# Kernel optimization log

Measured on AMD Instinct MI355X. Metric: run time of the kernel, lower is better.

Reference implementation:

```python
import jax, jax.numpy as jnp
import numpy as np

# dims matching init_kwargs
B, S, D, DH, E, K = 16, 8192, 256, 512, 8, 2


def setup_inputs() -> dict:
    key = jax.random.key(0)
    k0, k1, k2, k3 = jax.random.split(key, 4)
    scale = 0.02
    x = jax.random.normal(k0, (B, S, D), dtype=jnp.float32)
    gate_w = jax.random.normal(k1, (E, D), dtype=jnp.float32) * scale   # Linear(d_model, E, bias=False): weight [E, D]
    w1 = jax.random.normal(k2, (E, DH, D), dtype=jnp.float32) * scale   # fc1 weight per expert [DH, D]
    b1 = jnp.zeros((E, DH), dtype=jnp.float32)
    w2 = jax.random.normal(k3, (E, D, DH), dtype=jnp.float32) * scale   # fc2 weight per expert [D, DH]
    b2 = jnp.zeros((E, D), dtype=jnp.float32)
    return {"x": x, "gate_w": gate_w, "w1": w1, "b1": b1, "w2": w2, "b2": b2}


def reference(x, gate_w, w1, b1, w2, b2):
    b, s, d = x.shape
    e = gate_w.shape[0]
    xf = x.reshape(-1, d)                      # [T, D]
    T = xf.shape[0]

    # --- TopKRouter ---
    logits = xf @ gate_w.T                     # [T, E]
    probs = jax.nn.softmax(logits, axis=-1)
    topk_p, topk_i = jax.lax.top_k(probs, K)   # [T, K]
    topk_w = topk_p / topk_p.sum(axis=-1, keepdims=True)
    # load-balancing aux loss
    sel_mask = jax.nn.one_hot(topk_i, e, dtype=jnp.float32).sum(axis=1)  # [T, E]
    f_i = sel_mask.mean(axis=0)
    p_i = probs.mean(axis=0)
    aux_loss = e * jnp.sum(f_i * p_i)

    # --- dispatch: dense per-token expert weights (0 for unselected) ---
    dense_w = jnp.zeros((T, e), dtype=x.dtype).at[
        jnp.arange(T)[:, None], topk_i
    ].add(topk_w)                              # [T, E]

    # --- experts: loop over small fixed E; weight is zero for unselected tokens,
    # so this computes the same math as the sparse gather/scatter loop ---
    out = jnp.zeros_like(xf)
    for ei in range(e):
        h = jax.nn.silu(xf @ w1[ei].T + b1[ei])     # [T, DH]
        y = h @ w2[ei].T + b2[ei]                   # [T, D]
        out = out + dense_w[:, ei:ei + 1] * y

    return out.reshape(b, s, d), aux_loss
```

## Files before the change

### kernel.cpp

```cpp
#include <hip/hip_runtime.h>

typedef __attribute__((ext_vector_type(8))) short short8;
typedef __attribute__((ext_vector_type(4))) float f32x4;

#define T_TOK  131072
#define DMODEL 256
#define DHID   512
#define NEXP   8


__device__ __forceinline__ unsigned short f2bf(float f) {
  unsigned int u = __float_as_uint(f);
  u = (u + 0x7FFFu + ((u >> 16) & 1u)) >> 16;
  return (unsigned short)u;
}
__device__ __forceinline__ float bf2f(unsigned short u) {
  return __uint_as_float(((unsigned)u) << 16);
}

__device__ __forceinline__ void gload16(const void* g, void* l) {
  __builtin_amdgcn_global_load_lds(
      (const __attribute__((address_space(1))) void*)g,
      (__attribute__((address_space(3))) void*)l, 16, 0, 0);
}

__global__ void k_wconv(const float* __restrict__ w1, const float* __restrict__ w2,
                        const float* __restrict__ gate,
                        unsigned short* __restrict__ P1, unsigned short* __restrict__ P2,
                        double* __restrict__ gate_d) {
  int g = blockIdx.x * 256 + threadIdx.x;
  if (g < 2048) gate_d[g] = (double)gate[g];
  int e = g >> 14, rem = g & 16383;
  {
    int row = rem >> 5, c = rem & 31;
    int kc = c >> 3, cs = c & 7;
    const float* s = w1 + ((size_t)e * DHID + row) * DMODEL + c * 8;
    short8 v;
#pragma unroll
    for (int j = 0; j < 8; ++j) v[j] = (short)f2bf(s[j]);
    size_t dc = ((size_t)(e * 4 + kc) * 512 + row) * 8 + (cs ^ (row & 7));
    *(short8*)(P1 + dc * 8) = v;
  }
  {
    int row = rem >> 6, c = rem & 63;
    int kc = c >> 3, cs = c & 7;
    const float* s = w2 + ((size_t)e * DMODEL + row) * DHID + c * 8;
    short8 v;
#pragma unroll
    for (int j = 0; j < 8; ++j) v[j] = (short)f2bf(s[j]);
    size_t dc = ((size_t)(e * 8 + kc) * 256 + row) * 8 + (cs ^ (row & 7));
    *(short8*)(P2 + dc * 8) = v;
  }
}

__global__ __launch_bounds__(256, 2) void k_router(
    const float* __restrict__ x, const double* __restrict__ gd,
    unsigned short* __restrict__ xb, int* __restrict__ pack, float2* __restrict__ tkw,
    int* __restrict__ part_cnt, float* __restrict__ part_psum) {
  __shared__ float xs[16384];
  __shared__ double red[1024];
  __shared__ int s_cnt[NEXP];
  __shared__ float s_ps[NEXP];
  int tid = threadIdx.x;
  int tok = tid & 63, q = tid >> 6;
  int qu = __builtin_amdgcn_readfirstlane(q);

  for (int c = 0; c < 4; ++c) {
    if (tid < NEXP) { s_cnt[tid] = 0; s_ps[tid] = 0.f; }
    int tb = (blockIdx.x << 8) + (c << 6);
    __syncthreads();

#pragma unroll
    for (int i = 0; i < 16; ++i) {
      int idx = i * 256 + tid;
      int row = idx >> 6, c4 = (idx & 63) << 2;
      float4 v = *(const float4*)(x + (size_t)(tb + row) * 256 + c4);
      int sw = row & 31;
      float* xr = xs + row * 256;
      xr[(c4 + 0) ^ sw] = v.x;
      xr[(c4 + 1) ^ sw] = v.y;
      xr[(c4 + 2) ^ sw] = v.z;
      xr[(c4 + 3) ^ sw] = v.w;
      ushort4 u4;
      u4.x = f2bf(v.x); u4.y = f2bf(v.y); u4.z = f2bf(v.z); u4.w = f2bf(v.w);
      *(ushort4*)(xb + (size_t)(tb + row) * 256 + c4) = u4;
    }
    __syncthreads();

    double acc[8] = {0, 0, 0, 0, 0, 0, 0, 0};
    {
      int sw = tok & 31;
      const float* xr = xs + tok * 256;
#pragma unroll 4
      for (int d0 = 0; d0 < 64; ++d0) {
        int d = (qu << 6) + d0;
        double xv = (double)xr[d ^ sw];
#pragma unroll
        for (int e = 0; e < 8; ++e) acc[e] += xv * gd[e * 256 + d];
      }
    }

    double l[8];
#pragma unroll
    for (int j = 0; j < 4; ++j) red[tid * 4 + j] = acc[j];
    __syncthreads();
    if (tid < 64) {
#pragma unroll
      for (int j = 0; j < 4; ++j)
        l[j] = red[tid * 4 + j] + red[(64 + tid) * 4 + j] +
               red[(128 + tid) * 4 + j] + red[(192 + tid) * 4 + j];
    }
    __syncthreads();
#pragma unroll
    for (int j = 0; j < 4; ++j) red[tid * 4 + j] = acc[4 + j];
    __syncthreads();
    if (tid < 64) {
#pragma unroll
      for (int j = 0; j < 4; ++j)
        l[4 + j] = red[tid * 4 + j] + red[(64 + tid) * 4 + j] +
                   red[(128 + tid) * 4 + j] + red[(192 + tid) * 4 + j];
      int t = tb + tid;
      int i1 = 0;
#pragma unroll
      for (int e = 1; e < NEXP; ++e) if (l[e] > l[i1]) i1 = e;
      int i2 = (i1 == 0) ? 1 : 0;
#pragma unroll
      for (int e = 0; e < NEXP; ++e) if (e != i1 && l[e] > l[i2]) i2 = e;
      double m = l[0];
#pragma unroll
      for (int e = 1; e < NEXP; ++e) m = (l[e] > m) ? l[e] : m;
      float pe[NEXP]; float s = 0.f;
#pragma unroll
      for (int e = 0; e < NEXP; ++e) { pe[e] = __expf((float)(l[e] - m)); s += pe[e]; }
      float inv = 1.f / s;
      float p1 = pe[i1] * inv, p2 = pe[i2] * inv;
      float wn = 1.f / (p1 + p2);
      pack[t] = i1 | (i2 << 8);
      tkw[t] = make_float2(p1 * wn, p2 * wn);
      atomicAdd(&s_cnt[i1], 1); atomicAdd(&s_cnt[i2], 1);
#pragma unroll
      for (int e = 0; e < NEXP; ++e) atomicAdd(&s_ps[e], pe[e] * inv);
    }
    __syncthreads();
    if (tid < NEXP) {
      part_cnt[(blockIdx.x * 4 + c) * NEXP + tid] = s_cnt[tid];
      part_psum[(blockIdx.x * 4 + c) * NEXP + tid] = s_ps[tid];
    }
  }
}

__global__ __launch_bounds__(512) void k_scan(
    const int* __restrict__ part_cnt, const float* __restrict__ part_psum,
    int* __restrict__ block_off, int* __restrict__ cnt_total, float* __restrict__ out) {
  __shared__ float s_ps[NEXP];
  __shared__ int s_ct[NEXP];
  int lane = threadIdx.x & 63, wv = threadIdx.x >> 6;
  int base = lane * 32;
  int lsum = 0; float ps = 0.f;
#pragma unroll 8
  for (int j = 0; j < 32; ++j) {
    lsum += part_cnt[(base + j) * NEXP + wv];
    ps += part_psum[(base + j) * NEXP + wv];
  }
  int incl = lsum;
#pragma unroll
  for (int d = 1; d < 64; d <<= 1) { int t = __shfl_up(incl, d); if (lane >= d) incl += t; }
  int run = incl - lsum;
#pragma unroll 8
  for (int j = 0; j < 32; ++j) {
    int v = part_cnt[(base + j) * NEXP + wv];
    block_off[(base + j) * NEXP + wv] = run;
    run += v;
  }
#pragma unroll
  for (int d = 32; d; d >>= 1) ps += __shfl_xor(ps, d);
  int total = __shfl(incl, 63);
  if (lane == 0) { cnt_total[wv] = total; s_ct[wv] = total; s_ps[wv] = ps; }
  __syncthreads();
  if (threadIdx.x == 0) {
    double aux = 0.0; int rb = 0;
    for (int e = 0; e < NEXP; ++e) {
      aux += ((double)s_ct[e] / 131072.0) * ((double)s_ps[e] / 131072.0);
      cnt_total[8 + e] = rb;
      rb += (s_ct[e] + 255) & ~255;
    }
    out[33554432] = (float)(8.0 * aux);
  }
}

__global__ void k_scatter(const int* __restrict__ pack, float2* tkw,
                          const int* __restrict__ block_off, const int* __restrict__ cnt_total,
                          int* __restrict__ tok_list, float* __restrict__ wt_list) {
  __shared__ int s_loc[NEXP];
  int tid = threadIdx.x;
  if (tid < NEXP) s_loc[tid] = 0;
  __syncthreads();
  int t = (blockIdx.x << 6) + tid;
  int p = pack[t];
  float2 wv = tkw[t];
  int e1 = p & 255, e2 = (p >> 8) & 255;
  int o1 = block_off[blockIdx.x * NEXP + e1];
  int p1 = atomicAdd(&s_loc[e1], 1);
  int i1 = cnt_total[8 + e1] + o1 + p1;
  tok_list[i1] = t; wt_list[i1] = wv.x;
  int o2 = block_off[blockIdx.x * NEXP + e2];
  int p2 = atomicAdd(&s_loc[e2], 1);
  int i2 = cnt_total[8 + e2] + o2 + p2;
  tok_list[i2] = t; wt_list[i2] = wv.y;
  tkw[t] = make_float2(__int_as_float(i1), __int_as_float(i2));
}

__global__ __launch_bounds__(512, 2) void k_gemm1(
    const unsigned short* __restrict__ xb, const unsigned short* __restrict__ P1,
    const float* __restrict__ b1, const int* __restrict__ tok_list,
    const int* __restrict__ cnt_total, unsigned short* __restrict__ Hp) {
  __shared__ __align__(16) unsigned short buf[65536];
  __shared__ int s_tok[128];

  int bid = (blockIdx.x & 7) * 514 + (blockIdx.x >> 3);
  int e = -1, loc = 0, cum = 0, cnte = 0;
#pragma unroll
  for (int ee = 0; ee < NEXP; ++ee) {
    int ct = cnt_total[ee];
    int nb = ((ct + 127) >> 7) * 2;
    if (e < 0 && bid < cum + nb) { e = ee; loc = bid - cum; cnte = ct; }
    cum += nb;
  }
  if (e < 0) return;
  int mi = loc >> 1, ni = loc & 1;
  int nv = cnte - (mi << 7); if (nv > 128) nv = 128;
  int hbp = cnt_total[8 + e];

  int tid = threadIdx.x;
  int lane = tid & 63, w = tid >> 6, l15 = lane & 15, lg = lane >> 4;
  int wr = w >> 2, wc = w & 3;

  float b1v[4];
#pragma unroll
  for (int nt = 0; nt < 4; ++nt)
    b1v[nt] = b1[e * DHID + ni * 256 + wc * 64 + nt * 16 + l15];

  if (tid < 128) s_tok[tid] = tok_list[hbp + (mi << 7) + (tid < nv ? tid : nv - 1)];
  __syncthreads();

  int ar0 = tid >> 5;
  int ac = tid & 31;
#pragma unroll
  for (int i = 0; i < 8; ++i) {
    int row = i * 16 + ar0;
    gload16(xb + (size_t)s_tok[row] * DMODEL + (size_t)((ac ^ (row & 7)) << 3),
            &buf[(size_t)(i * 512 + w * 64) * 8]);
  }
  auto stage_b = [&](int kc) {
    const unsigned short* src = P1 + ((size_t)(e * 4 + kc) * 512 + ni * 256) * 64;
    int d = 32768 + (kc & 1) * 16384;
#pragma unroll
    for (int i = 0; i < 4; ++i) {
      int cidx = i * 512 + tid;
      gload16(src + (size_t)cidx * 8, &buf[d + (i * 512 + w * 64) * 8]);
    }
  };
  stage_b(0);
  asm volatile("s_waitcnt vmcnt(0)" ::: "memory");
  __builtin_amdgcn_s_barrier();
  __builtin_amdgcn_sched_barrier(0);

  int aidx[4][2], bidx[4][2];
#pragma unroll
  for (int mt = 0; mt < 4; ++mt) {
    int r = wr * 64 + mt * 16 + l15, r7 = r & 7;
#pragma unroll
    for (int ks = 0; ks < 2; ++ks) aidx[mt][ks] = r * 256 + (((ks * 4 + lg) ^ r7) << 3);
  }
#pragma unroll
  for (int nt = 0; nt < 4; ++nt) {
    int r = wc * 64 + nt * 16 + l15, r7 = r & 7;
#pragma unroll
    for (int ks = 0; ks < 2; ++ks) bidx[nt][ks] = r * 64 + (((ks * 4 + lg) ^ r7) << 3);
  }

  f32x4 acc[4][4];
#pragma unroll
  for (int mt = 0; mt < 4; ++mt)
#pragma unroll
    for (int nt = 0; nt < 4; ++nt) acc[mt][nt] = (f32x4){0.f, 0.f, 0.f, 0.f};

  for (int s = 0; s < 4; ++s) {
    if (s < 3) stage_b(s + 1);
    int abase = s * 64;
    int bbase = 32768 + (s & 1) * 16384;
#pragma unroll
    for (int ks = 0; ks < 2; ++ks) {
      short8 a[4], b[4];
#pragma unroll
      for (int mt = 0; mt < 4; ++mt) a[mt] = *(const short8*)&buf[abase + aidx[mt][ks]];
#pragma unroll
      for (int nt = 0; nt < 4; ++nt) b[nt] = *(const short8*)&buf[bbase + bidx[nt][ks]];
#pragma unroll
      for (int mt = 0; mt < 4; ++mt)
#pragma unroll
        for (int nt = 0; nt < 4; ++nt)
          acc[mt][nt] = __builtin_amdgcn_mfma_f32_16x16x32_bf16(a[mt], b[nt], acc[mt][nt], 0, 0, 0);
    }
    asm volatile("s_waitcnt vmcnt(0)" ::: "memory");
    __builtin_amdgcn_s_barrier();
    __builtin_amdgcn_sched_barrier(0);
  }

#pragma unroll
  for (int mt = 0; mt < 4; ++mt) {
    int rbase0 = (wr * 64 + mt * 16) * 264;
#pragma unroll
    for (int nt = 0; nt < 4; ++nt) {
      int col = wc * 64 + nt * 16 + l15;
      int c3 = col >> 3, c7 = col & 7;
#pragma unroll
      for (int rr = 0; rr < 4; ++rr) {
        int lr = lg * 4 + rr;
        int r7 = lr & 7;
        int p = (c3 & 24) | ((c3 & 7) ^ r7);
        float z = acc[mt][nt][rr] + b1v[nt];
        float sv = z * __builtin_amdgcn_rcpf(1.f + __expf(-z));
        buf[rbase0 + lr * 264 + (p << 3) + c7] =
            (unsigned short)(__float_as_uint(sv) >> 16);
      }
    }
  }
  __syncthreads();
  {
    int blk = (hbp >> 8) + (mi >> 1);
    int rbase = (mi & 1) * 128;
    int kc_l = w >> 1, half = w & 1;
    int rl = lane >> 3, sl = lane & 7;
    unsigned short* pdst =
        Hp + ((size_t)(blk * 8 + ni * 4 + kc_l) * 256 + rbase + half * 64) * 64;
    short8 z8 = {0, 0, 0, 0, 0, 0, 0, 0};
#pragma unroll
    for (int j = 0; j < 8; ++j) {
      int r = half * 64 + j * 8 + rl;
      short8 v = (r < nv) ? *(const short8*)&buf[r * 264 + ((kc_l * 8 + sl) << 3)] : z8;
      *(short8*)&pdst[(size_t)(j * 8 + rl) * 64 + sl * 8] = v;
    }
  }
}

__global__ __launch_bounds__(512, 2) void k_gemm2c(
    unsigned short* Hp, const unsigned short* __restrict__ P2,
    const float* __restrict__ b2, const float* __restrict__ wt_list,
    const int* __restrict__ cnt_total) {
  __shared__ __align__(16) unsigned short buf[65536];
  __shared__ float s_wt[256];

  int bid = (blockIdx.x & 7) * 129 + (blockIdx.x >> 3);
  int e = -1, mi = 0, cum = 0, cnte = 0;
#pragma unroll
  for (int ee = 0; ee < NEXP; ++ee) {
    int ct = cnt_total[ee];
    int nb = (ct + 255) >> 8;
    if (e < 0 && bid < cum + nb) { e = ee; mi = bid - cum; cnte = ct; }
    cum += nb;
  }
  if (e < 0) return;
  int nv = cnte - (mi << 8); if (nv > 256) nv = 256;
  int hbp = cnt_total[8 + e];
  int blk = (hbp >> 8) + mi;

  int tid = threadIdx.x;
  int lane = tid & 63, w = tid >> 6, l15 = lane & 15, lg = lane >> 4;
  int wr = w >> 2, wc = w & 3;

  float b2v[4];
#pragma unroll
  for (int nt = 0; nt < 4; ++nt)
    b2v[nt] = b2[e * DMODEL + wc * 64 + nt * 16 + l15];

  if (tid < 256) s_wt[tid] = (tid < nv) ? wt_list[hbp + (mi << 8) + tid] : 0.f;
  __syncthreads();

  auto stage = [&](int s) {
    int d = (s & 1) * 32768;
    const unsigned short* sa = Hp + (size_t)(blk * 8 + s) * 16384;
    const unsigned short* sb = P2 + (size_t)(e * 8 + s) * 16384;
#pragma unroll
    for (int i = 0; i < 4; ++i) {
      int c = i * 512 + tid;
      gload16(sa + (size_t)c * 8, &buf[d + (i * 512 + w * 64) * 8]);
    }
#pragma unroll
    for (int i = 0; i < 4; ++i) {
      int c = i * 512 + tid;
      gload16(sb + (size_t)c * 8, &buf[d + 16384 + (i * 512 + w * 64) * 8]);
    }
  };

  int aidx[8][2], bidx[4][2];
#pragma unroll
  for (int mt = 0; mt < 8; ++mt) {
    int r = wr * 128 + mt * 16 + l15, r7 = r & 7;
#pragma unroll
    for (int ks = 0; ks < 2; ++ks) aidx[mt][ks] = r * 64 + (((ks * 4 + lg) ^ r7) << 3);
  }
#pragma unroll
  for (int nt = 0; nt < 4; ++nt) {
    int r = wc * 64 + nt * 16 + l15, r7 = r & 7;
#pragma unroll
    for (int ks = 0; ks < 2; ++ks) bidx[nt][ks] = r * 64 + (((ks * 4 + lg) ^ r7) << 3);
  }

  f32x4 acc[8][4];
#pragma unroll
  for (int mt = 0; mt < 8; ++mt)
#pragma unroll
    for (int nt = 0; nt < 4; ++nt) acc[mt][nt] = (f32x4){0.f, 0.f, 0.f, 0.f};

  stage(0);
  asm volatile("s_waitcnt vmcnt(0)" ::: "memory");
  __builtin_amdgcn_s_barrier();
  __builtin_amdgcn_sched_barrier(0);

  for (int s = 0; s < 8; ++s) {
    if (s < 7) stage(s + 1);
    int ab = (s & 1) * 32768, bb = ab + 16384;
#pragma unroll
    for (int ks = 0; ks < 2; ++ks) {
      short8 a[8], b[4];
#pragma unroll
      for (int mt = 0; mt < 8; ++mt) a[mt] = *(const short8*)&buf[ab + aidx[mt][ks]];
#pragma unroll
      for (int nt = 0; nt < 4; ++nt) b[nt] = *(const short8*)&buf[bb + bidx[nt][ks]];
#pragma unroll
      for (int mt = 0; mt < 8; ++mt)
#pragma unroll
        for (int nt = 0; nt < 4; ++nt)
          acc[mt][nt] = __builtin_amdgcn_mfma_f32_16x16x32_bf16(a[mt], b[nt], acc[mt][nt], 0, 0, 0);
    }
    asm volatile("s_waitcnt vmcnt(0)" ::: "memory");
    __builtin_amdgcn_s_barrier();
    __builtin_amdgcn_sched_barrier(0);
  }

#pragma unroll
  for (int mt = 0; mt < 8; ++mt) {
    int rbase0 = (wr * 128 + mt * 16) * 256;
#pragma unroll
    for (int nt = 0; nt < 4; ++nt) {
      int col = wc * 64 + nt * 16 + l15;
#pragma unroll
      for (int rr = 0; rr < 4; ++rr) {
        int row = wr * 128 + mt * 16 + lg * 4 + rr;
        float v = s_wt[row] * (acc[mt][nt][rr] + b2v[nt]);
        buf[rbase0 + (lg * 4 + rr) * 256 + col] =
            (unsigned short)(__float_as_uint(v) >> 16);
      }
    }
  }
  __syncthreads();
  unsigned short* ydst = Hp + (size_t)blk * 131072;
#pragma unroll
  for (int i = 0; i < 16; ++i) {
    size_t cidx = (size_t)(i * 512 + tid) * 8;
    *(short8*)&ydst[cidx] = *(const short8*)&buf[cidx];
  }
}

__global__ __launch_bounds__(256) void k_reduce(
    const unsigned short* __restrict__ Y, const float2* __restrict__ inv,
    float* __restrict__ out) {
  int g = blockIdx.x * 256 + threadIdx.x;
#pragma unroll
  for (int it = 0; it < 8; ++it) {
    int t = g >> 5;
    int cw = (g & 31) << 3;
    float2 iv = inv[t];
    int s1 = __float_as_int(iv.x), s2 = __float_as_int(iv.y);
    const unsigned short* y1 = Y + (size_t)(s1 >> 8) * 131072 + (size_t)(s1 & 255) * 256 + cw;
    const unsigned short* y2 = Y + (size_t)(s2 >> 8) * 131072 + (size_t)(s2 & 255) * 256 + cw;
    short8 a = *(const short8*)y1;
    short8 b = *(const short8*)y2;
    float* op = out + (size_t)t * 256 + cw;
    float4 r0, r1;
    r0.x = bf2f((unsigned short)a[0]) + bf2f((unsigned short)b[0]);
    r0.y = bf2f((unsigned short)a[1]) + bf2f((unsigned short)b[1]);
    r0.z = bf2f((unsigned short)a[2]) + bf2f((unsigned short)b[2]);
    r0.w = bf2f((unsigned short)a[3]) + bf2f((unsigned short)b[3]);
    r1.x = bf2f((unsigned short)a[4]) + bf2f((unsigned short)b[4]);
    r1.y = bf2f((unsigned short)a[5]) + bf2f((unsigned short)b[5]);
    r1.z = bf2f((unsigned short)a[6]) + bf2f((unsigned short)b[6]);
    r1.w = bf2f((unsigned short)a[7]) + bf2f((unsigned short)b[7]);
    *(float4*)op = r0;
    *(float4*)(op + 4) = r1;
    g += 2048 * 256;
  }
}

extern "C" void kernel_launch(void* const* d_in, const int* in_sizes, int n_in,
                              void* d_out, int out_size, void* d_ws, size_t ws_size,
                              hipStream_t stream) {
  const float* x    = (const float*)d_in[0];
  const float* gate = (const float*)d_in[1];
  const float* w1   = (const float*)d_in[2];
  const float* b1   = (const float*)d_in[3];
  const float* w2   = (const float*)d_in[4];
  const float* b2   = (const float*)d_in[5];
  float* out = (float*)d_out;
  char* ws = (char*)d_ws;

  unsigned short* xb  = (unsigned short*)(ws);
  unsigned short* P1  = (unsigned short*)(ws + 67108864);
  unsigned short* P2  = (unsigned short*)(ws + 69206016);
  int*    tok_list  = (int*)(ws + 71303168);
  float*  wt_list   = (float*)(ws + 72368128);
  int*    pack      = (int*)(ws + 73433088);
  float2* tkw       = (float2*)(ws + 73957376);
  int*    part_cnt  = (int*)(ws + 75005952);
  float*  part_psum = (float*)(ws + 75071488);
  int*    block_off = (int*)(ws + 75137024);
  int*    cnt_total = (int*)(ws + 75202560);
  double* gate_d    = (double*)(ws + 75235328);
  unsigned short* Hp = (unsigned short*)(ws + 75497472);

  k_wconv<<<512, 256, 0, stream>>>(w1, w2, gate, P1, P2, gate_d);
  k_router<<<512, 256, 0, stream>>>(x, gate_d, xb, pack, tkw, part_cnt, part_psum);
  k_scan<<<1, 512, 0, stream>>>(part_cnt, part_psum, block_off, cnt_total, out);
  k_scatter<<<2048, 64, 0, stream>>>(pack, tkw, block_off, cnt_total, tok_list, wt_list);
  k_gemm1<<<4112, 512, 0, stream>>>(xb, P1, b1, tok_list, cnt_total, Hp);
  k_gemm2c<<<1032, 512, 0, stream>>>(Hp, P2, b2, wt_list, cnt_total);
  k_reduce<<<2048, 256, 0, stream>>>(Hp, tkw, out);
}
```

Measured before the change: 508.6 us.

## Narrow gemm1 N-tile to 128 and stream A per k-chunk to halve LDS

The first expert GEMM kernel now computes 128x128 output tiles instead of 128x256, launching twice as many blocks. The gathered token rows of A are no longer preloaded in full; they are double-buffered per 64-wide k chunk together with B, which cuts LDS per block from 128KB to 64KB. The aim is to allow more resident blocks per CU and better latency hiding. In exchange, each token row is gathered twice as often and there are fewer MFMAs per LDS read, lowering arithmetic intensity.

```diff
diff --git a/kernel.cpp b/kernel.cpp
--- a/kernel.cpp
+++ b/kernel.cpp
@@ -214,20 +214,20 @@
     const unsigned short* __restrict__ xb, const unsigned short* __restrict__ P1,
     const float* __restrict__ b1, const int* __restrict__ tok_list,
     const int* __restrict__ cnt_total, unsigned short* __restrict__ Hp) {
-  __shared__ __align__(16) unsigned short buf[65536];
+  __shared__ __align__(16) unsigned short buf[32768];
   __shared__ int s_tok[128];
 
-  int bid = (blockIdx.x & 7) * 514 + (blockIdx.x >> 3);
+  int bid = (blockIdx.x & 7) * 1029 + (blockIdx.x >> 3);
   int e = -1, loc = 0, cum = 0, cnte = 0;
 #pragma unroll
   for (int ee = 0; ee < NEXP; ++ee) {
     int ct = cnt_total[ee];
-    int nb = ((ct + 127) >> 7) * 2;
+    int nb = ((ct + 127) >> 7) * 4;
     if (e < 0 && bid < cum + nb) { e = ee; loc = bid - cum; cnte = ct; }
     cum += nb;
   }
   if (e < 0) return;
-  int mi = loc >> 1, ni = loc & 1;
+  int mi = loc >> 2, ni = loc & 3;
   int nv = cnte - (mi << 7); if (nv > 128) nv = 128;
   int hbp = cnt_total[8 + e];
 
@@ -235,71 +235,75 @@
   int lane = tid & 63, w = tid >> 6, l15 = lane & 15, lg = lane >> 4;
   int wr = w >> 2, wc = w & 3;
 
-  float b1v[4];
-#pragma unroll
-  for (int nt = 0; nt < 4; ++nt)
-    b1v[nt] = b1[e * DHID + ni * 256 + wc * 64 + nt * 16 + l15];
+  float b1v[2];
+#pragma unroll
+  for (int nt = 0; nt < 2; ++nt)
+    b1v[nt] = b1[e * DHID + ni * 128 + wc * 32 + nt * 16 + l15];
 
   if (tid < 128) s_tok[tid] = tok_list[hbp + (mi << 7) + (tid < nv ? tid : nv - 1)];
   __syncthreads();
 
-  int ar0 = tid >> 5;
-  int ac = tid & 31;
-#pragma unroll
-  for (int i = 0; i < 8; ++i) {
-    int row = i * 16 + ar0;
-    gload16(xb + (size_t)s_tok[row] * DMODEL + (size_t)((ac ^ (row & 7)) << 3),
-            &buf[(size_t)(i * 512 + w * 64) * 8]);
-  }
-  auto stage_b = [&](int kc) {
-    const unsigned short* src = P1 + ((size_t)(e * 4 + kc) * 512 + ni * 256) * 64;
-    int d = 32768 + (kc & 1) * 16384;
-#pragma unroll
-    for (int i = 0; i < 4; ++i) {
-      int cidx = i * 512 + tid;
-      gload16(src + (size_t)cidx * 8, &buf[d + (i * 512 + w * 64) * 8]);
+  int arow0 = tid >> 3, acs = tid & 7;
+  const unsigned short* pa[2];
+#pragma unroll
+  for (int i = 0; i < 2; ++i) {
+    int row = i * 64 + arow0;
+    pa[i] = xb + (size_t)s_tok[row] * DMODEL + ((acs ^ (row & 7)) << 3);
+  }
+  const unsigned short* pb = P1 + ((size_t)(e * 4) * 512 + ni * 128) * 64;
+
+  auto stage = [&](int kc) {
+    int ab = (kc & 1) * 8192, bb = 16384 + (kc & 1) * 8192;
+#pragma unroll
+    for (int i = 0; i < 2; ++i)
+      gload16(pa[i] + kc * 64, &buf[(size_t)(ab + (i * 512 + w * 64) * 8)]);
+    const unsigned short* src = pb + (size_t)kc * 32768;
+#pragma unroll
+    for (int i = 0; i < 2; ++i) {
+      int c = i * 512 + tid;
+      gload16(src + (size_t)c * 8, &buf[(size_t)(bb + (i * 512 + w * 64) * 8)]);
     }
   };
-  stage_b(0);
+
+  int aidx[4][2], bidx[2][2];
+#pragma unroll
+  for (int mt = 0; mt < 4; ++mt) {
+    int r = wr * 64 + mt * 16 + l15, r7 = r & 7;
+#pragma unroll
+    for (int ks = 0; ks < 2; ++ks) aidx[mt][ks] = r * 64 + (((ks * 4 + lg) ^ r7) << 3);
+  }
+#pragma unroll
+  for (int nt = 0; nt < 2; ++nt) {
+    int r = wc * 32 + nt * 16 + l15, r7 = r & 7;
+#pragma unroll
+    for (int ks = 0; ks < 2; ++ks) bidx[nt][ks] = r * 64 + (((ks * 4 + lg) ^ r7) << 3);
+  }
+
+  f32x4 acc[4][2];
+#pragma unroll
+  for (int mt = 0; mt < 4; ++mt)
+#pragma unroll
+    for (int nt = 0; nt < 2; ++nt) acc[mt][nt] = (f32x4){0.f, 0.f, 0.f, 0.f};
+
+  stage(0);
   asm volatile("s_waitcnt vmcnt(0)" ::: "memory");
   __builtin_amdgcn_s_barrier();
   __builtin_amdgcn_sched_barrier(0);
 
-  int aidx[4][2], bidx[4][2];
-#pragma unroll
-  for (int mt = 0; mt < 4; ++mt) {
-    int r = wr * 64 + mt * 16 + l15, r7 = r & 7;
-#pragma unroll
-    for (int ks = 0; ks < 2; ++ks) aidx[mt][ks] = r * 256 + (((ks * 4 + lg) ^ r7) << 3);
-  }
-#pragma unroll
-  for (int nt = 0; nt < 4; ++nt) {
-    int r = wc * 64 + nt * 16 + l15, r7 = r & 7;
-#pragma unroll
-    for (int ks = 0; ks < 2; ++ks) bidx[nt][ks] = r * 64 + (((ks * 4 + lg) ^ r7) << 3);
-  }
-
-  f32x4 acc[4][4];
-#pragma unroll
-  for (int mt = 0; mt < 4; ++mt)
-#pragma unroll
-    for (int nt = 0; nt < 4; ++nt) acc[mt][nt] = (f32x4){0.f, 0.f, 0.f, 0.f};
-
   for (int s = 0; s < 4; ++s) {
-    if (s < 3) stage_b(s + 1);
-    int abase = s * 64;
-    int bbase = 32768 + (s & 1) * 16384;
+    if (s < 3) stage(s + 1);
+    int ab = (s & 1) * 8192, bb = 16384 + (s & 1) * 8192;
 #pragma unroll
     for (int ks = 0; ks < 2; ++ks) {
-      short8 a[4], b[4];
-#pragma unroll
-      for (int mt = 0; mt < 4; ++mt) a[mt] = *(const short8*)&buf[abase + aidx[mt][ks]];
-#pragma unroll
-      for (int nt = 0; nt < 4; ++nt) b[nt] = *(const short8*)&buf[bbase + bidx[nt][ks]];
+      short8 a[4], b[2];
+#pragma unroll
+      for (int mt = 0; mt < 4; ++mt) a[mt] = *(const short8*)&buf[ab + aidx[mt][ks]];
+#pragma unroll
+      for (int nt = 0; nt < 2; ++nt) b[nt] = *(const short8*)&buf[bb + bidx[nt][ks]];
 #pragma unroll
       for (int mt = 0; mt < 4; ++mt)
 #pragma unroll
-        for (int nt = 0; nt < 4; ++nt)
+        for (int nt = 0; nt < 2; ++nt)
           acc[mt][nt] = __builtin_amdgcn_mfma_f32_16x16x32_bf16(a[mt], b[nt], acc[mt][nt], 0, 0, 0);
     }
     asm volatile("s_waitcnt vmcnt(0)" ::: "memory");
@@ -309,19 +313,19 @@
 
 #pragma unroll
   for (int mt = 0; mt < 4; ++mt) {
-    int rbase0 = (wr * 64 + mt * 16) * 264;
-#pragma unroll
-    for (int nt = 0; nt < 4; ++nt) {
-      int col = wc * 64 + nt * 16 + l15;
+    int rbase0 = (wr * 64 + mt * 16) * 128;
+#pragma unroll
+    for (int nt = 0; nt < 2; ++nt) {
+      int col = wc * 32 + nt * 16 + l15;
       int c3 = col >> 3, c7 = col & 7;
 #pragma unroll
       for (int rr = 0; rr < 4; ++rr) {
         int lr = lg * 4 + rr;
         int r7 = lr & 7;
-        int p = (c3 & 24) | ((c3 & 7) ^ r7);
+        int p = (c3 & 8) | ((c3 & 7) ^ r7);
         float z = acc[mt][nt][rr] + b1v[nt];
         float sv = z * __builtin_amdgcn_rcpf(1.f + __expf(-z));
-        buf[rbase0 + lr * 264 + (p << 3) + c7] =
+        buf[rbase0 + lr * 128 + (p << 3) + c7] =
             (unsigned short)(__float_as_uint(sv) >> 16);
       }
     }
@@ -330,16 +334,14 @@
   {
     int blk = (hbp >> 8) + (mi >> 1);
     int rbase = (mi & 1) * 128;
-    int kc_l = w >> 1, half = w & 1;
-    int rl = lane >> 3, sl = lane & 7;
-    unsigned short* pdst =
-        Hp + ((size_t)(blk * 8 + ni * 4 + kc_l) * 256 + rbase + half * 64) * 64;
     short8 z8 = {0, 0, 0, 0, 0, 0, 0, 0};
 #pragma unroll
-    for (int j = 0; j < 8; ++j) {
-      int r = half * 64 + j * 8 + rl;
-      short8 v = (r < nv) ? *(const short8*)&buf[r * 264 + ((kc_l * 8 + sl) << 3)] : z8;
-      *(short8*)&pdst[(size_t)(j * 8 + rl) * 64 + sl * 8] = v;
+    for (int i = 0; i < 4; ++i) {
+      int t = i * 512 + tid;
+      int row = t >> 4, s = t & 15;
+      short8 v = (row < nv) ? *(const short8*)&buf[row * 128 + s * 8] : z8;
+      size_t dc = ((size_t)(blk * 8 + ni * 2 + (s >> 3)) * 256 + rbase + row) * 8 + (s & 7);
+      *(short8*)&Hp[dc * 8] = v;
     }
   }
 }
@@ -523,7 +525,7 @@
   k_router<<<512, 256, 0, stream>>>(x, gate_d, xb, pack, tkw, part_cnt, part_psum);
   k_scan<<<1, 512, 0, stream>>>(part_cnt, part_psum, block_off, cnt_total, out);
   k_scatter<<<2048, 64, 0, stream>>>(pack, tkw, block_off, cnt_total, tok_list, wt_list);
-  k_gemm1<<<4112, 512, 0, stream>>>(xb, P1, b1, tok_list, cnt_total, Hp);
+  k_gemm1<<<8232, 512, 0, stream>>>(xb, P1, b1, tok_list, cnt_total, Hp);
   k_gemm2c<<<1032, 512, 0, stream>>>(Hp, P2, b2, wt_list, cnt_total);
   k_reduce<<<2048, 256, 0, stream>>>(Hp, tkw, out);
 }
```

Measured after the change: 484.4 us, median of 2. 1.05x faster.
